# Kernel optimization log

Hardware: AMD Instinct MI355X
Metric: run time of the kernel (lower is better)

Reference implementation:

```python
import jax, jax.numpy as jnp
import numpy as np

K = 5            # srn kernel size (kernels[0])
EPSILON = 1e-3   # epsilons -> SRN additive noise scale
BN_EPS = 1e-5
NUM_SLICES = 3
OUT_CH = 64
CLASSES = 5


def _unfold(x, k):
    # torch.nn.Unfold, padding=0: (B, C*k*k, L), channel-major then (kh, kw) row-major
    B, C, H, W = x.shape
    Ho, Wo = H - k + 1, W - k + 1
    cols = jnp.stack([x[:, :, i:i + Ho, j:j + Wo]
                      for i in range(k) for j in range(k)], axis=2)  # (B,C,k*k,Ho,Wo)
    return cols.reshape(B, C * k * k, Ho * Wo), Ho, Wo


def _bn(x, g, b):
    # BatchNorm2d in training mode: batch statistics, biased variance
    m = x.mean((0, 2, 3), keepdims=True)
    v = x.var((0, 2, 3), keepdims=True)
    return (x - m) * jax.lax.rsqrt(v + BN_EPS) * g[None, :, None, None] + b[None, :, None, None]


def _conv(x, w, b):
    y = jax.lax.conv_general_dilated(x, w, (1, 1), 'VALID',
                                     dimension_numbers=('NCHW', 'OIHW', 'NCHW'))
    return y + b[None, :, None, None]


def _avgpool(x, s):
    B, C, H, W = x.shape
    return x.reshape(B, C, H // s, s, W // s, s).mean((3, 5))


def _maxpool(x, s):
    B, C, H, W = x.shape
    return x.reshape(B, C, H // s, s, W // s, s).max((3, 5))


def _srn(x, srn_w):
    B = x.shape[0]
    y, Ho, Wo = _unfold(x, K)                               # (B, n, L)
    y = y + EPSILON * jax.random.normal(jax.random.key(42), y.shape, y.dtype)
    gg = jnp.std(y, axis=1, ddof=1, keepdims=True)          # torch.std is unbiased
    y = y / gg
    O, C, _, _, S = srn_w.shape
    n = C * K * K
    X = srn_w.reshape(O, n, S)
    X = jnp.concatenate([jnp.ones((O, n, 1), X.dtype), X], axis=2)   # (O, n, S+1)
    Xcov = jnp.einsum('onf,ong->ofg', X, X)                 # X^T X, (O, 4, 4)
    Xinv = jnp.linalg.inv(Xcov)
    M = jnp.einsum('ofg,ong->ofn', Xinv, X)
    Wc = jnp.einsum('ofn,bnl->bofl', M, y)
    pred = jnp.einsum('onf,bofl->bonl', X, Wc)              # fitted values (B,O,n,L)
    err = jnp.mean((y[:, None] - pred) ** 2, axis=2)        # (B,O,L)
    err = err.reshape(B, O, Ho, Wo)
    A = (jnp.exp(-err) - np.exp(-1.0)) / (1.0 - np.exp(-1.0))
    return A - 0.5


def setup_inputs() -> dict:
    key = jax.random.key(0)
    ks = jax.random.split(key, 12)
    x = jax.random.normal(ks[0], (4, 3, 64, 64), jnp.float32)
    # xavier-style init scaled up for numerical stability of the small-matrix inverse
    srn_w = 0.05 * jax.random.normal(ks[1], (OUT_CH, 3, K, K, NUM_SLICES), jnp.float32)
    conv2_w = 0.05 * jax.random.normal(ks[2], (128, 64, 3, 3), jnp.float32)
    conv2_b = 0.01 * jax.random.normal(ks[3], (128,), jnp.float32)
    conv3_w = 0.05 * jax.random.normal(ks[4], (128, 128, 3, 3), jnp.float32)
    conv3_b = 0.01 * jax.random.normal(ks[5], (128,), jnp.float32)
    conv4_w = 0.05 * jax.random.normal(ks[6], (128, 128, 3, 3), jnp.float32)
    conv4_b = 0.01 * jax.random.normal(ks[7], (128,), jnp.float32)
    bn1_g = jnp.ones((64,), jnp.float32); bn1_b = jnp.zeros((64,), jnp.float32)
    bn2_g = jnp.ones((128,), jnp.float32); bn2_b = jnp.zeros((128,), jnp.float32)
    bn3_g = jnp.ones((128,), jnp.float32); bn3_b = jnp.zeros((128,), jnp.float32)
    bn4_g = jnp.ones((128,), jnp.float32); bn4_b = jnp.zeros((128,), jnp.float32)
    fc2_w = 0.05 * jax.random.normal(ks[8], (CLASSES, 128, 1, 1), jnp.float32)
    fc2_b = 0.01 * jax.random.normal(ks[9], (CLASSES,), jnp.float32)
    return dict(x=x, srn_w=srn_w, conv2_w=conv2_w, conv2_b=conv2_b,
                conv3_w=conv3_w, conv3_b=conv3_b, conv4_w=conv4_w, conv4_b=conv4_b,
                bn1_g=bn1_g, bn1_b=bn1_b, bn2_g=bn2_g, bn2_b=bn2_b,
                bn3_g=bn3_g, bn3_b=bn3_b, bn4_g=bn4_g, bn4_b=bn4_b,
                fc2_w=fc2_w, fc2_b=fc2_b)


def reference(x, srn_w, conv2_w, conv2_b, conv3_w, conv3_b, conv4_w, conv4_b,
              bn1_g, bn1_b, bn2_g, bn2_b, bn3_g, bn3_b, bn4_g, bn4_b,
              fc2_w, fc2_b):
    h = _srn(x, srn_w)                                      # (B,64,60,60)
    h = _avgpool(h, 2)
    h = _bn(h, bn1_g, bn1_b)
    h = jax.nn.relu(_bn(_conv(h, conv2_w, conv2_b), bn2_g, bn2_b))
    h = _avgpool(h, 2)
    h = jax.nn.relu(_bn(_conv(h, conv3_w, conv3_b), bn3_g, bn3_b))
    h = _maxpool(h, 2)
    h = jax.nn.relu(_bn(_conv(h, conv4_w, conv4_b), bn4_g, bn4_b))
    h = _maxpool(h, 4)                                      # (B,128,1,1)
    flat = h.reshape(h.shape[0], -1)                        # (B,128)
    return flat @ fc2_w.reshape(CLASSES, -1).T + fc2_b      # 1x1 conv == matmul
```

## Files before the change

### kernel.cpp

```cpp
#include <hip/hip_runtime.h>
#include <math.h>

__device__ __align__(16) float g_w2p[16 * 1152 * 4];
__device__ __align__(16) float g_w3p[32 * 1152 * 4];
__device__ __align__(16) float g_w4p[8 * 4608 * 4];
__device__ __align__(16) float g_h1[4 * 30 * 30 * 64];
__device__ __align__(16) float g_h2[4 * 14 * 14 * 4 * 128];
__device__ __align__(16) float g_h3[4 * 6 * 6 * 4 * 128];
__device__ __align__(16) float g_h4[4 * 16 * 128];

__global__ __launch_bounds__(256) void k_srn(const float* __restrict__ x,
                                             const float* __restrict__ srn_w,
                                             const float* __restrict__ w2,
                                             float* __restrict__ stats) {
    __shared__ __align__(16) float wlds[64 * 244];
    __shared__ float xsm[648];
    __shared__ float part[2 * 15 * 66];
    __shared__ float redS[256], redQ[256];
    int bid = blockIdx.x, t = threadIdx.x;
    int b = bid / 60, rem = bid % 60, r = rem >> 1, ch = rem & 1;

    for (int j = bid * 256 + t; j < 73728; j += 240 * 256) {
        int c = j & 3, s4 = j >> 2;
        int sl = s4 % 36, tmp = s4 / 36, oc_l = tmp & 31, blk = tmp >> 5;
        int it = blk & 3, ocg = blk >> 2;
        int kw = sl % 3, icq = (sl / 3) & 3, kh = sl / 12;
        int ic = it * 16 + icq * 4 + c;
        g_w2p[j] = w2[((ocg * 32 + oc_l) * 64 + ic) * 9 + kh * 3 + kw];
    }

    float4 wr[15];
#pragma unroll
    for (int k = 0; k < 15; k++) {
        int i4 = k * 256 + t;
        if (i4 < 3600) wr[k] = ((const float4*)srn_w)[i4];
    }
    float xr[3];
#pragma unroll
    for (int k = 0; k < 3; k++) {
        int i = t + k * 256;
        if (i < 648) {
            int c = i / 216, rm = i % 216, rr = rm / 36, col = rm % 36;
            int gc = ch * 30 + col; if (gc > 63) gc = 63;
            xr[k] = x[((b * 3 + c) * 64 + (2 * r + rr)) * 64 + gc];
        }
    }
#pragma unroll
    for (int k = 0; k < 15; k++) {
        int i4 = k * 256 + t;
        if (i4 < 3600) {
            float v4[4] = { wr[k].x, wr[k].y, wr[k].z, wr[k].w };
#pragma unroll
            for (int e = 0; e < 4; e++) {
                int i = i4 * 4 + e, o = i / 225, jj = i % 225;
                wlds[o * 244 + (jj / 15) * 16 + (jj % 15)] = v4[e];
            }
        }
    }
#pragma unroll
    for (int k = 0; k < 3; k++) { int i = t + k * 256; if (i < 648) xsm[i] = xr[k]; }
    __syncthreads();

    int w = t >> 6, o = t & 63;
    int rw = w & 1, cq = w >> 1, base = cq * 16;

    float z1[16], z2[16], z3[16], s[16], q[16];
#pragma unroll
    for (int i = 0; i < 16; i++) { z1[i]=0; z2[i]=0; z3[i]=0; s[i]=0; q[i]=0; }

    for (int c = 0; c < 3; c++) {
#pragma unroll
        for (int kh = 0; kh < 5; kh++) {
            float xv[20];
#pragma unroll
            for (int k = 0; k < 20; k++) xv[k] = xsm[(c * 6 + rw + kh) * 36 + base + k];
            float wf[16];
            const float* wp = &wlds[o * 244 + (c * 5 + kh) * 16];
            *(float4*)&wf[0]  = *(const float4*)&wp[0];
            *(float4*)&wf[4]  = *(const float4*)&wp[4];
            *(float4*)&wf[8]  = *(const float4*)&wp[8];
            *(float4*)&wf[12] = *(const float4*)&wp[12];
#pragma unroll
            for (int kw = 0; kw < 5; kw++) {
                float w1 = wf[kw * 3], w2v = wf[kw * 3 + 1], w3v = wf[kw * 3 + 2];
#pragma unroll
                for (int i = 0; i < 16; i++) {
                    float v = xv[kw + i];
                    s[i] += v; q[i] += v * v;
                    z1[i] += w1 * v; z2[i] += w2v * v; z3[i] += w3v * v;
                }
            }
        }
    }

    float gm[16];
    {
        float c01=0,c02=0,c03=0,c11=0,c12=0,c13=0,c22=0,c23=0,c33=0;
#pragma unroll
        for (int row = 0; row < 15; row++) {
            float wf[16];
            const float* wp = &wlds[o * 244 + row * 16];
            *(float4*)&wf[0]  = *(const float4*)&wp[0];
            *(float4*)&wf[4]  = *(const float4*)&wp[4];
            *(float4*)&wf[8]  = *(const float4*)&wp[8];
            *(float4*)&wf[12] = *(const float4*)&wp[12];
#pragma unroll
            for (int kw = 0; kw < 5; kw++) {
                float w1 = wf[kw*3], w2v = wf[kw*3+1], w3v = wf[kw*3+2];
                c01 += w1; c02 += w2v; c03 += w3v;
                c11 += w1*w1; c12 += w1*w2v; c13 += w1*w3v;
                c22 += w2v*w2v; c23 += w2v*w3v; c33 += w3v*w3v;
            }
        }
        float A[4][8];
        A[0][0]=75.f; A[0][1]=c01; A[0][2]=c02; A[0][3]=c03;
        A[1][0]=c01;  A[1][1]=c11; A[1][2]=c12; A[1][3]=c13;
        A[2][0]=c02;  A[2][1]=c12; A[2][2]=c22; A[2][3]=c23;
        A[3][0]=c03;  A[3][1]=c13; A[3][2]=c23; A[3][3]=c33;
#pragma unroll
        for (int i = 0; i < 4; i++)
#pragma unroll
            for (int j = 0; j < 4; j++) A[i][4 + j] = (i == j) ? 1.f : 0.f;
#pragma unroll
        for (int p = 0; p < 4; p++) {
            float ip = 1.f / A[p][p];
#pragma unroll
            for (int j = 0; j < 8; j++) A[p][j] *= ip;
#pragma unroll
            for (int i = 0; i < 4; i++) if (i != p) {
                float f = A[i][p];
#pragma unroll
                for (int j = 0; j < 8; j++) A[i][j] -= f * A[p][j];
            }
        }
#pragma unroll
        for (int i = 0; i < 4; i++)
#pragma unroll
            for (int j = 0; j < 4; j++) gm[i * 4 + j] = A[i][4 + j];
    }

    const float C1 = 0.36787944117144233f;
    const float INV = 1.5819767068693265f;
#pragma unroll
    for (int pp = 0; pp < 8; pp++) {
        int pl = cq * 8 + pp;
        if (pl < 15) {
            float aa = 0.f;
#pragma unroll
            for (int e = 0; e < 2; e++) {
                int i = 2 * pp + e;
                float sum = s[i], sq = q[i];
                float gg2 = (sq - sum * sum * (1.f / 75.f)) * (1.f / 74.f);
                float zf[4] = { sum, z1[i], z2[i], z3[i] };
                float qf = 0.f;
#pragma unroll
                for (int f = 0; f < 4; f++) {
                    float acc = 0.f;
#pragma unroll
                    for (int h = 0; h < 4; h++) acc += gm[f * 4 + h] * zf[h];
                    qf += acc * zf[f];
                }
                float err = (sq - qf) / (75.f * gg2);
                aa += (expf(-err) - C1) * INV - 0.5f;
            }
            part[(rw * 15 + pl) * 66 + o] = 0.25f * aa;
        }
    }
    __syncthreads();

    int j2 = t >> 6;
    float ps = 0.f, pq = 0.f;
    for (int pl = j2; pl < 15; pl += 4) {
        float v = part[pl * 66 + o] + part[(15 + pl) * 66 + o];
        g_h1[((b * 30 + r) * 30 + ch * 15 + pl) * 64 + o] = v;
        ps += v; pq += v * v;
    }
    redS[t] = ps; redQ[t] = pq;
    __syncthreads();
    if (t < 64) {
        atomicAdd(&stats[t],      redS[t] + redS[64 + t] + redS[128 + t] + redS[192 + t]);
        atomicAdd(&stats[64 + t], redQ[t] + redQ[64 + t] + redQ[128 + t] + redQ[192 + t]);
    }
}

__global__ __launch_bounds__(256) void k_conv2(const float* __restrict__ w3,
                                               const float* __restrict__ g1,
                                               const float* __restrict__ b1,
                                               float* __restrict__ stats) {
    __shared__ __align__(16) float ws[2 * 32 * 148];
    __shared__ __align__(16) float xs[3 * 16 * 64];
    __shared__ float redS[256], redQ[256];
    int blk = blockIdx.x, t = threadIdx.x;
    int b = blk / 224, rem = blk % 224, oh = rem >> 3, sub = rem & 7;
    int owh = sub >> 2, ocg = sub & 3;
    int oc_l = t & 31, grp = t >> 5;
    int now = (grp < 6) ? 2 : 1;
    int lowb = (grp < 6) ? grp * 2 : 12 + (grp - 6);

    {
        int j = blk * 256 + t;
        if (j < 147456) {
            int c = j & 3, s4 = j >> 2;
            int sl = s4 % 36, tmp = s4 / 36, oc2 = tmp & 31, bk = tmp >> 5;
            int it = bk & 7, og = bk >> 3;
            int kw = sl % 3, icq = (sl / 3) & 3, kh = sl / 12;
            int ic = it * 16 + icq * 4 + c;
            g_w3p[j] = w3[((og * 32 + oc2) * 128 + ic) * 9 + kh * 3 + kw];
        }
    }

    const float4* wsrc = (const float4*)g_w2p + (ocg * 4) * 1152;
    {
        int icb = (t & 15) * 4;
        float4 S = *(const float4*)&stats[icb], Q = *(const float4*)&stats[64 + icb];
        float4 G4 = *(const float4*)&g1[icb], B4 = *(const float4*)&b1[icb];
        float scv[4], shv[4];
        float mm[4] = { S.x, S.y, S.z, S.w }, qq[4] = { Q.x, Q.y, Q.z, Q.w };
        float gg[4] = { G4.x, G4.y, G4.z, G4.w }, bb[4] = { B4.x, B4.y, B4.z, B4.w };
#pragma unroll
        for (int c = 0; c < 4; c++) {
            float m = mm[c] * (1.f / 3600.f);
            float v = qq[c] * (1.f / 3600.f) - m * m;
            scv[c] = gg[c] * rsqrtf(v + 1e-5f);
            shv[c] = bb[c] - m * scv[c];
        }
        int px = t >> 4, ic4 = t & 15;
        float4 xr[3];
#pragma unroll
        for (int k = 0; k < 3; k++)
            xr[k] = ((const float4*)g_h1)[((b * 30 + oh + k) * 30 + owh * 14 + px) * 16 + ic4];
        float4 wreg[9];
#pragma unroll
        for (int k = 0; k < 9; k++) wreg[k] = wsrc[k * 256 + t];
#pragma unroll
        for (int k = 0; k < 3; k++) {
            float4 v;
            v.x = xr[k].x * scv[0] + shv[0]; v.y = xr[k].y * scv[1] + shv[1];
            v.z = xr[k].z * scv[2] + shv[2]; v.w = xr[k].w * scv[3] + shv[3];
            *(float4*)&xs[((k * 16 + px) * 16 + ic4) * 4] = v;
        }
#pragma unroll
        for (int k = 0; k < 9; k++) {
            int idx = k * 256 + t;
            int tile = idx / 1152, r2 = idx % 1152;
            *(float4*)&ws[tile * 4736 + (r2 / 36) * 148 + (r2 % 36) * 4] = wreg[k];
        }
    }
    __syncthreads();

    float acc[2] = {0, 0};
    for (int rr = 0; rr < 2; ++rr) {
        float4 wreg[9];
        if (rr == 0) {
#pragma unroll
            for (int k = 0; k < 9; k++) wreg[k] = wsrc[2 * 1152 + k * 256 + t];
        }
        for (int half = 0; half < 2; ++half) {
            int it = rr * 2 + half;
            const float* wB = &ws[half * 4736 + oc_l * 148];
#pragma unroll 1
            for (int icq = 0; icq < 4; icq++) {
                int xoff = it * 16 + icq * 4;
#pragma unroll
                for (int kh = 0; kh < 3; kh++) {
                    const float* wb = &wB[(kh * 4 + icq) * 12];
                    float4 w0 = *(const float4*)&wb[0];
                    float4 w1 = *(const float4*)&wb[4];
                    float4 w2v = *(const float4*)&wb[8];
                    const float* xrow = &xs[(kh * 16 + lowb) * 64 + xoff];
                    float4 x0 = *(const float4*)&xrow[0];
                    float4 x1 = *(const float4*)&xrow[64];
#pragma unroll
                    for (int i = 0; i < 2; i++) {
                        if (i < now) {
                            float4 x2 = *(const float4*)&xrow[(i + 2) * 64];
                            acc[i] += w0.x * x0.x + w0.y * x0.y + w0.z * x0.z + w0.w * x0.w
                                    + w1.x * x1.x + w1.y * x1.y + w1.z * x1.z + w1.w * x1.w
                                    + w2v.x * x2.x + w2v.y * x2.y + w2v.z * x2.z + w2v.w * x2.w;
                            x0 = x1; x1 = x2;
                        }
                    }
                }
            }
        }
        if (rr == 0) {
            __syncthreads();
#pragma unroll
            for (int k = 0; k < 9; k++) {
                int idx = k * 256 + t;
                int tile = idx / 1152, r2 = idx % 1152;
                *(float4*)&ws[tile * 4736 + (r2 / 36) * 148 + (r2 % 36) * 4] = wreg[k];
            }
            __syncthreads();
        }
    }
    int oc = ocg * 32 + oc_l;
    float ps = 0.f, pq = 0.f;
#pragma unroll
    for (int i = 0; i < 2; i++) {
        if (i < now) {
            int ow = owh * 14 + lowb + i;
            g_h2[(((b * 14 + (oh >> 1)) * 14 + (ow >> 1)) * 4 + (oh & 1) * 2 + (ow & 1)) * 128 + oc] = acc[i];
            ps += acc[i]; pq += acc[i] * acc[i];
        }
    }
    redS[t] = ps; redQ[t] = pq;
    __syncthreads();
    if (t < 32) {
        float aS = 0.f, aQ = 0.f;
#pragma unroll
        for (int k = 0; k < 8; k++) { aS += redS[t + 32 * k]; aQ += redQ[t + 32 * k]; }
        atomicAdd(&stats[128 + ocg * 32 + t], aS);
        atomicAdd(&stats[256 + ocg * 32 + t], aQ);
    }
}

__global__ __launch_bounds__(256) void k_conv3(const float* __restrict__ w4,
                                               const float* __restrict__ g2,
                                               const float* __restrict__ b2,
                                               float* __restrict__ stats) {
    __shared__ __align__(16) float ws[2 * 32 * 148];
    __shared__ __align__(16) float xs[3 * 14 * 128];
    __shared__ float redS[256], redQ[256];
    int blk = blockIdx.x, t = threadIdx.x;
    int b = blk / 48, rem = blk % 48, oh = rem >> 2, ocg = rem & 3;
    int oc_l = t & 31, grp = t >> 5;
    int now = (grp < 4) ? 2 : 1;
    int lowb = (grp < 4) ? grp * 2 : 8 + (grp - 4);

    for (int j = blk * 256 + t; j < 147456; j += 192 * 256) {
        int c = j & 3, s4 = j >> 2;
        int sl = s4 % 72, tmp = s4 / 72, oc2 = tmp & 15, blkq = tmp >> 4;
        int icq = blkq & 3, og = blkq >> 2;
        int kw = sl % 3, icb2 = (sl / 3) & 7, kh = sl / 24;
        int ic = icq * 32 + icb2 * 4 + c;
        g_w4p[j] = w4[((og * 16 + oc2) * 128 + ic) * 9 + kh * 3 + kw];
    }

    const float4* wsrc = (const float4*)g_w3p + (ocg * 8) * 1152;
    {
        int icb = (t & 31) * 4;
        float4 S = *(const float4*)&stats[128 + icb], Q = *(const float4*)&stats[256 + icb];
        float4 G4 = *(const float4*)&g2[icb], B4 = *(const float4*)&b2[icb];
        float scv[4], shv[4];
        float mm[4] = { S.x, S.y, S.z, S.w }, qq[4] = { Q.x, Q.y, Q.z, Q.w };
        float gg[4] = { G4.x, G4.y, G4.z, G4.w }, bb[4] = { B4.x, B4.y, B4.z, B4.w };
#pragma unroll
        for (int c = 0; c < 4; c++) {
            float m = mm[c] * (1.f / 3136.f);
            float v = qq[c] * (1.f / 3136.f) - m * m;
            scv[c] = gg[c] * rsqrtf(v + 1e-5f);
            shv[c] = bb[c] - m * scv[c];
        }
        float4 wreg[9];
#pragma unroll
        for (int k = 0; k < 9; k++) wreg[k] = wsrc[k * 256 + t];
        float4 pa[6], pb[6], pc[6], pd[6];
#pragma unroll
        for (int k = 0; k < 6; k++) {
            int i4 = t + k * 256;
            if (i4 < 1344) {
                int px = (i4 >> 5) % 14, rr2 = i4 / 448;
                const float4* p0 = (const float4*)&g_h2[(((b * 14 + oh + rr2) * 14 + px) * 4) * 128 + (i4 & 31) * 4];
                pa[k] = p0[0]; pb[k] = p0[32]; pc[k] = p0[64]; pd[k] = p0[96];
            }
        }
#pragma unroll
        for (int k = 0; k < 9; k++) {
            int idx = k * 256 + t;
            int tile = idx / 1152, r2 = idx % 1152;
            *(float4*)&ws[tile * 4736 + (r2 / 36) * 148 + (r2 % 36) * 4] = wreg[k];
        }
#pragma unroll
        for (int k = 0; k < 6; k++) {
            int i4 = t + k * 256;
            if (i4 < 1344) {
                float4 o4;
                o4.x = 0.25f * (fmaxf(pa[k].x * scv[0] + shv[0], 0.f) + fmaxf(pb[k].x * scv[0] + shv[0], 0.f)
                              + fmaxf(pc[k].x * scv[0] + shv[0], 0.f) + fmaxf(pd[k].x * scv[0] + shv[0], 0.f));
                o4.y = 0.25f * (fmaxf(pa[k].y * scv[1] + shv[1], 0.f) + fmaxf(pb[k].y * scv[1] + shv[1], 0.f)
                              + fmaxf(pc[k].y * scv[1] + shv[1], 0.f) + fmaxf(pd[k].y * scv[1] + shv[1], 0.f));
                o4.z = 0.25f * (fmaxf(pa[k].z * scv[2] + shv[2], 0.f) + fmaxf(pb[k].z * scv[2] + shv[2], 0.f)
                              + fmaxf(pc[k].z * scv[2] + shv[2], 0.f) + fmaxf(pd[k].z * scv[2] + shv[2], 0.f));
                o4.w = 0.25f * (fmaxf(pa[k].w * scv[3] + shv[3], 0.f) + fmaxf(pb[k].w * scv[3] + shv[3], 0.f)
                              + fmaxf(pc[k].w * scv[3] + shv[3], 0.f) + fmaxf(pd[k].w * scv[3] + shv[3], 0.f));
                *(float4*)&xs[i4 * 4] = o4;
            }
        }
    }
    __syncthreads();

    float acc[2] = {0, 0};
    for (int rr = 0; rr < 4; ++rr) {
        float4 wreg[9];
        if (rr < 3) {
#pragma unroll
            for (int k = 0; k < 9; k++) wreg[k] = wsrc[(2 * rr + 2) * 1152 + k * 256 + t];
        }
        for (int half = 0; half < 2; ++half) {
            int it = rr * 2 + half;
            const float* wB = &ws[half * 4736 + oc_l * 148];
#pragma unroll 1
            for (int icq = 0; icq < 4; icq++) {
                int xoff = it * 16 + icq * 4;
#pragma unroll
                for (int kh = 0; kh < 3; kh++) {
                    const float* wb = &wB[(kh * 4 + icq) * 12];
                    float4 w0 = *(const float4*)&wb[0];
                    float4 w1 = *(const float4*)&wb[4];
                    float4 w2v = *(const float4*)&wb[8];
                    const float* xrow = &xs[(kh * 14 + lowb) * 128 + xoff];
                    float4 x0 = *(const float4*)&xrow[0];
                    float4 x1 = *(const float4*)&xrow[128];
#pragma unroll
                    for (int i = 0; i < 2; i++) {
                        if (i < now) {
                            float4 x2 = *(const float4*)&xrow[(i + 2) * 128];
                            acc[i] += w0.x * x0.x + w0.y * x0.y + w0.z * x0.z + w0.w * x0.w
                                    + w1.x * x1.x + w1.y * x1.y + w1.z * x1.z + w1.w * x1.w
                                    + w2v.x * x2.x + w2v.y * x2.y + w2v.z * x2.z + w2v.w * x2.w;
                            x0 = x1; x1 = x2;
                        }
                    }
                }
            }
        }
        if (rr < 3) {
            __syncthreads();
#pragma unroll
            for (int k = 0; k < 9; k++) {
                int idx = k * 256 + t;
                int tile = idx / 1152, r2 = idx % 1152;
                *(float4*)&ws[tile * 4736 + (r2 / 36) * 148 + (r2 % 36) * 4] = wreg[k];
            }
            __syncthreads();
        }
    }
    int oc = ocg * 32 + oc_l;
    float ps = 0.f, pq = 0.f;
#pragma unroll
    for (int i = 0; i < 2; i++) {
        if (i < now) {
            int ow = lowb + i;
            g_h3[(((b * 6 + (oh >> 1)) * 6 + (ow >> 1)) * 4 + (oh & 1) * 2 + (ow & 1)) * 128 + oc] = acc[i];
            ps += acc[i]; pq += acc[i] * acc[i];
        }
    }
    redS[t] = ps; redQ[t] = pq;
    __syncthreads();
    if (t < 32) {
        float aS = 0.f, aQ = 0.f;
#pragma unroll
        for (int k = 0; k < 8; k++) { aS += redS[t + 32 * k]; aQ += redQ[t + 32 * k]; }
        atomicAdd(&stats[384 + ocg * 32 + t], aS);
        atomicAdd(&stats[512 + ocg * 32 + t], aQ);
    }
}

__global__ __launch_bounds__(256) void k_conv4(const float* __restrict__ g3,
                                               const float* __restrict__ b3,
                                               float* __restrict__ stats) {
    __shared__ __align__(16) float ws[64 * 292];
    __shared__ __align__(16) float xs[3 * 6 * 128];
    __shared__ float red[256];
    int blk = blockIdx.x, t = threadIdx.x;
    int b = blk / 32, rem = blk % 32, oh = rem / 8, ocg = rem % 8;
    int oc_l = t & 15, ow = (t >> 4) & 3, icq = t >> 6;

    {
        int icb = (t & 31) * 4;
        float4 S = *(const float4*)&stats[384 + icb], Q = *(const float4*)&stats[512 + icb];
        float4 G4 = *(const float4*)&g3[icb], B4 = *(const float4*)&b3[icb];
        float scv[4], shv[4];
        float mm[4] = { S.x, S.y, S.z, S.w }, qq[4] = { Q.x, Q.y, Q.z, Q.w };
        float gg[4] = { G4.x, G4.y, G4.z, G4.w }, bb[4] = { B4.x, B4.y, B4.z, B4.w };
#pragma unroll
        for (int c = 0; c < 4; c++) {
            float m = mm[c] * (1.f / 576.f);
            float v = qq[c] * (1.f / 576.f) - m * m;
            scv[c] = gg[c] * rsqrtf(v + 1e-5f);
            shv[c] = bb[c] - m * scv[c];
        }
        const float4* wsrc = (const float4*)g_w4p + ocg * 4608;
        float4 wreg[18];
#pragma unroll
        for (int k = 0; k < 18; k++) wreg[k] = wsrc[k * 256 + t];
        float4 pa[3], pb[3], pc[3], pd[3];
#pragma unroll
        for (int k = 0; k < 3; k++) {
            int i4 = t + k * 256;
            if (i4 < 576) {
                int px = (i4 >> 5) % 6, rr = i4 / 192;
                const float4* p0 = (const float4*)&g_h3[(((b * 6 + oh + rr) * 6 + px) * 4) * 128 + (i4 & 31) * 4];
                pa[k] = p0[0]; pb[k] = p0[32]; pc[k] = p0[64]; pd[k] = p0[96];
            }
        }
#pragma unroll
        for (int k = 0; k < 18; k++) {
            int idx = k * 256 + t;
            *(float4*)&ws[(idx / 72) * 292 + (idx % 72) * 4] = wreg[k];
        }
#pragma unroll
        for (int k = 0; k < 3; k++) {
            int i4 = t + k * 256;
            if (i4 < 576) {
                float4 o4;
                o4.x = fmaxf(fmaxf(fmaxf(pa[k].x * scv[0] + shv[0], pb[k].x * scv[0] + shv[0]),
                                   fmaxf(pc[k].x * scv[0] + shv[0], pd[k].x * scv[0] + shv[0])), 0.f);
                o4.y = fmaxf(fmaxf(fmaxf(pa[k].y * scv[1] + shv[1], pb[k].y * scv[1] + shv[1]),
                                   fmaxf(pc[k].y * scv[1] + shv[1], pd[k].y * scv[1] + shv[1])), 0.f);
                o4.z = fmaxf(fmaxf(fmaxf(pa[k].z * scv[2] + shv[2], pb[k].z * scv[2] + shv[2]),
                                   fmaxf(pc[k].z * scv[2] + shv[2], pd[k].z * scv[2] + shv[2])), 0.f);
                o4.w = fmaxf(fmaxf(fmaxf(pa[k].w * scv[3] + shv[3], pb[k].w * scv[3] + shv[3]),
                                   fmaxf(pc[k].w * scv[3] + shv[3], pd[k].w * scv[3] + shv[3])), 0.f);
                *(float4*)&xs[i4 * 4] = o4;
            }
        }
    }
    __syncthreads();

    float acc = 0.f;
    const float* wbase = &ws[(icq * 16 + oc_l) * 292];
#pragma unroll 1
    for (int icbq = 0; icbq < 8; icbq++) {
#pragma unroll
        for (int kh = 0; kh < 3; kh++) {
            const float* wb = &wbase[(kh * 8 + icbq) * 12];
            float4 w0 = *(const float4*)&wb[0];
            float4 w1 = *(const float4*)&wb[4];
            float4 w2v = *(const float4*)&wb[8];
            float4 x0 = *(const float4*)&xs[(kh * 6 + ow) * 128 + icq * 32 + icbq * 4];
            float4 x1 = *(const float4*)&xs[(kh * 6 + ow + 1) * 128 + icq * 32 + icbq * 4];
            float4 x2 = *(const float4*)&xs[(kh * 6 + ow + 2) * 128 + icq * 32 + icbq * 4];
            acc += w0.x * x0.x + w0.y * x0.y + w0.z * x0.z + w0.w * x0.w
                 + w1.x * x1.x + w1.y * x1.y + w1.z * x1.z + w1.w * x1.w
                 + w2v.x * x2.x + w2v.y * x2.y + w2v.z * x2.z + w2v.w * x2.w;
        }
    }
    red[t] = acc;
    __syncthreads();
    if (t < 64) {
        float v = red[t] + red[t + 64] + red[t + 128] + red[t + 192];
        int oc = ocg * 16 + (t & 15);
        g_h4[((b * 4 + oh) * 4 + (t >> 4)) * 128 + oc] = v;
        float ps = v + __shfl_xor(v, 16);  ps += __shfl_xor(ps, 32);
        float pv = v * v;
        float pq = pv + __shfl_xor(pv, 16); pq += __shfl_xor(pq, 32);
        if (t < 16) {
            atomicAdd(&stats[640 + ocg * 16 + t], ps);
            atomicAdd(&stats[768 + ocg * 16 + t], pq);
        }
    }
}

__global__ __launch_bounds__(256) void k_final(const float* __restrict__ g4,
                                               const float* __restrict__ b4,
                                               const float* __restrict__ fcw,
                                               const float* __restrict__ fcb,
                                               const float* __restrict__ stats,
                                               float* __restrict__ out) {
    __shared__ float sc[128], sh[128];
    __shared__ float pooled[4][128];
    int t = threadIdx.x;
    if (t < 128) {
        float m = stats[640 + t] * (1.f / 64.f);
        float v = stats[768 + t] * (1.f / 64.f) - m * m;
        float rs = rsqrtf(v + 1e-5f);
        sc[t] = g4[t] * rs; sh[t] = b4[t] - m * sc[t];
    }
    __syncthreads();
    for (int item = t; item < 512; item += 256) {
        int bb = item >> 7, oc = item & 127;
        float s = sc[oc], h = sh[oc];
        float mx = 0.f;
#pragma unroll
        for (int k = 0; k < 16; k++) mx = fmaxf(mx, g_h4[(bb * 16 + k) * 128 + oc] * s + h);
        pooled[bb][oc] = mx;
    }
    __syncthreads();
    if (t < 20) {
        int bb = t / 5, cls = t % 5;
        float acc = fcb[cls];
        const float* w = &fcw[cls * 128];
        for (int oc = 0; oc < 128; oc++) acc += pooled[bb][oc] * w[oc];
        out[bb * 5 + cls] = acc;
    }
}

extern "C" void kernel_launch(void* const* d_in, const int* in_sizes, int n_in,
                              void* d_out, int out_size, void* d_ws, size_t ws_size,
                              hipStream_t stream) {
    (void)in_sizes; (void)n_in; (void)out_size; (void)ws_size;
    const float* x     = (const float*)d_in[0];
    const float* srn_w = (const float*)d_in[1];
    const float* w2    = (const float*)d_in[2];
    const float* w3    = (const float*)d_in[4];
    const float* w4    = (const float*)d_in[6];
    const float* g1 = (const float*)d_in[8];  const float* b1 = (const float*)d_in[9];
    const float* g2 = (const float*)d_in[10]; const float* b2 = (const float*)d_in[11];
    const float* g3 = (const float*)d_in[12]; const float* b3 = (const float*)d_in[13];
    const float* g4 = (const float*)d_in[14]; const float* b4 = (const float*)d_in[15];
    const float* fcw = (const float*)d_in[16]; const float* fcb = (const float*)d_in[17];
    float* out = (float*)d_out;
    float* stats = (float*)d_ws;

    hipMemsetAsync(d_ws, 0, 4096, stream);
    k_srn  <<<dim3(240), dim3(256), 0, stream>>>(x, srn_w, w2, stats);
    k_conv2<<<dim3(896), dim3(256), 0, stream>>>(w3, g1, b1, stats);
    k_conv3<<<dim3(192), dim3(256), 0, stream>>>(w4, g2, b2, stats);
    k_conv4<<<dim3(128), dim3(256), 0, stream>>>(g3, b3, stats);
    k_final<<<dim3(1),   dim3(256), 0, stream>>>(g4, b4, fcw, fcb, stats, out);
}
```

Before: 102.3 us.

## Split conv3 input-channel reduction across two thread halves and fold final into conv4

```diff
diff --git a/kernel.cpp b/kernel.cpp
--- a/kernel.cpp
+++ b/kernel.cpp
@@ -315,20 +315,21 @@
     }
 }
 
-__global__ __launch_bounds__(256) void k_conv3(const float* __restrict__ w4,
+__global__ __launch_bounds__(512) void k_conv3(const float* __restrict__ w4,
                                                const float* __restrict__ g2,
                                                const float* __restrict__ b2,
                                                float* __restrict__ stats) {
     __shared__ __align__(16) float ws[2 * 32 * 148];
     __shared__ __align__(16) float xs[3 * 14 * 128];
-    __shared__ float redS[256], redQ[256];
+    __shared__ float accr[512 * 2];
+    __shared__ float redS[512], redQ[512];
     int blk = blockIdx.x, t = threadIdx.x;
     int b = blk / 48, rem = blk % 48, oh = rem >> 2, ocg = rem & 3;
-    int oc_l = t & 31, grp = t >> 5;
+    int oc_l = t & 31, icqh = (t >> 5) & 1, grp = t >> 6;
     int now = (grp < 4) ? 2 : 1;
     int lowb = (grp < 4) ? grp * 2 : 8 + (grp - 4);
 
-    for (int j = blk * 256 + t; j < 147456; j += 192 * 256) {
+    for (int j = blk * 512 + t; j < 147456; j += 192 * 512) {
         int c = j & 3, s4 = j >> 2;
         int sl = s4 % 72, tmp = s4 / 72, oc2 = tmp & 15, blkq = tmp >> 4;
         int icq = blkq & 3, og = blkq >> 2;
@@ -352,13 +353,13 @@
             scv[c] = gg[c] * rsqrtf(v + 1e-5f);
             shv[c] = bb[c] - m * scv[c];
         }
-        float4 wreg[9];
-#pragma unroll
-        for (int k = 0; k < 9; k++) wreg[k] = wsrc[k * 256 + t];
-        float4 pa[6], pb[6], pc[6], pd[6];
-#pragma unroll
-        for (int k = 0; k < 6; k++) {
-            int i4 = t + k * 256;
+        float4 wreg[5];
+#pragma unroll
+        for (int k = 0; k < 5; k++) { int i4 = k * 512 + t; if (i4 < 2304) wreg[k] = wsrc[i4]; }
+        float4 pa[3], pb[3], pc[3], pd[3];
+#pragma unroll
+        for (int k = 0; k < 3; k++) {
+            int i4 = t + k * 512;
             if (i4 < 1344) {
                 int px = (i4 >> 5) % 14, rr2 = i4 / 448;
                 const float4* p0 = (const float4*)&g_h2[(((b * 14 + oh + rr2) * 14 + px) * 4) * 128 + (i4 & 31) * 4];
@@ -366,14 +367,16 @@
             }
         }
 #pragma unroll
-        for (int k = 0; k < 9; k++) {
-            int idx = k * 256 + t;
-            int tile = idx / 1152, r2 = idx % 1152;
-            *(float4*)&ws[tile * 4736 + (r2 / 36) * 148 + (r2 % 36) * 4] = wreg[k];
-        }
-#pragma unroll
-        for (int k = 0; k < 6; k++) {
-            int i4 = t + k * 256;
+        for (int k = 0; k < 5; k++) {
+            int i4 = k * 512 + t;
+            if (i4 < 2304) {
+                int tile = i4 / 1152, r2 = i4 % 1152;
+                *(float4*)&ws[tile * 4736 + (r2 / 36) * 148 + (r2 % 36) * 4] = wreg[k];
+            }
+        }
+#pragma unroll
+        for (int k = 0; k < 3; k++) {
+            int i4 = t + k * 512;
             if (i4 < 1344) {
                 float4 o4;
                 o4.x = 0.25f * (fmaxf(pa[k].x * scv[0] + shv[0], 0.f) + fmaxf(pb[k].x * scv[0] + shv[0], 0.f)
@@ -392,16 +395,17 @@
 
     float acc[2] = {0, 0};
     for (int rr = 0; rr < 4; ++rr) {
-        float4 wreg[9];
+        float4 wreg[5];
         if (rr < 3) {
 #pragma unroll
-            for (int k = 0; k < 9; k++) wreg[k] = wsrc[(2 * rr + 2) * 1152 + k * 256 + t];
+            for (int k = 0; k < 5; k++) { int i4 = k * 512 + t; if (i4 < 2304) wreg[k] = wsrc[(2 * rr + 2) * 1152 + i4]; }
         }
         for (int half = 0; half < 2; ++half) {
             int it = rr * 2 + half;
             const float* wB = &ws[half * 4736 + oc_l * 148];
 #pragma unroll 1
-            for (int icq = 0; icq < 4; icq++) {
+            for (int iq = 0; iq < 2; iq++) {
+                int icq = icqh * 2 + iq;
                 int xoff = it * 16 + icq * 4;
 #pragma unroll
                 for (int kh = 0; kh < 3; kh++) {
@@ -428,22 +432,31 @@
         if (rr < 3) {
             __syncthreads();
 #pragma unroll
-            for (int k = 0; k < 9; k++) {
-                int idx = k * 256 + t;
-                int tile = idx / 1152, r2 = idx % 1152;
-                *(float4*)&ws[tile * 4736 + (r2 / 36) * 148 + (r2 % 36) * 4] = wreg[k];
+            for (int k = 0; k < 5; k++) {
+                int i4 = k * 512 + t;
+                if (i4 < 2304) {
+                    int tile = i4 / 1152, r2 = i4 % 1152;
+                    *(float4*)&ws[tile * 4736 + (r2 / 36) * 148 + (r2 % 36) * 4] = wreg[k];
+                }
             }
             __syncthreads();
         }
     }
-    int oc = ocg * 32 + oc_l;
+    accr[t * 2]     = acc[0];
+    accr[t * 2 + 1] = acc[1];
+    __syncthreads();
     float ps = 0.f, pq = 0.f;
-#pragma unroll
-    for (int i = 0; i < 2; i++) {
-        if (i < now) {
-            int ow = lowb + i;
-            g_h3[(((b * 6 + (oh >> 1)) * 6 + (ow >> 1)) * 4 + (oh & 1) * 2 + (ow & 1)) * 128 + oc] = acc[i];
-            ps += acc[i]; pq += acc[i] * acc[i];
+    if (icqh == 0) {
+        acc[0] += accr[(t + 32) * 2];
+        acc[1] += accr[(t + 32) * 2 + 1];
+        int oc = ocg * 32 + oc_l;
+#pragma unroll
+        for (int i = 0; i < 2; i++) {
+            if (i < now) {
+                int ow = lowb + i;
+                g_h3[(((b * 6 + (oh >> 1)) * 6 + (ow >> 1)) * 4 + (oh & 1) * 2 + (ow & 1)) * 128 + oc] = acc[i];
+                ps += acc[i]; pq += acc[i] * acc[i];
+            }
         }
     }
     redS[t] = ps; redQ[t] = pq;
@@ -451,7 +464,7 @@
     if (t < 32) {
         float aS = 0.f, aQ = 0.f;
 #pragma unroll
-        for (int k = 0; k < 8; k++) { aS += redS[t + 32 * k]; aQ += redQ[t + 32 * k]; }
+        for (int k = 0; k < 16; k++) { aS += redS[t + 32 * k]; aQ += redQ[t + 32 * k]; }
         atomicAdd(&stats[384 + ocg * 32 + t], aS);
         atomicAdd(&stats[512 + ocg * 32 + t], aQ);
     }
@@ -459,7 +472,12 @@
 
 __global__ __launch_bounds__(256) void k_conv4(const float* __restrict__ g3,
                                                const float* __restrict__ b3,
-                                               float* __restrict__ stats) {
+                                               const float* __restrict__ g4,
+                                               const float* __restrict__ b4,
+                                               const float* __restrict__ fcw,
+                                               const float* __restrict__ fcb,
+                                               float* __restrict__ stats,
+                                               float* __restrict__ out) {
     __shared__ __align__(16) float ws[64 * 292];
     __shared__ __align__(16) float xs[3 * 6 * 128];
     __shared__ float red[256];
@@ -551,39 +569,41 @@
             atomicAdd(&stats[768 + ocg * 16 + t], pq);
         }
     }
-}
-
-__global__ __launch_bounds__(256) void k_final(const float* __restrict__ g4,
-                                               const float* __restrict__ b4,
-                                               const float* __restrict__ fcw,
-                                               const float* __restrict__ fcb,
-                                               const float* __restrict__ stats,
-                                               float* __restrict__ out) {
-    __shared__ float sc[128], sh[128];
-    __shared__ float pooled[4][128];
-    int t = threadIdx.x;
-    if (t < 128) {
-        float m = stats[640 + t] * (1.f / 64.f);
-        float v = stats[768 + t] * (1.f / 64.f) - m * m;
-        float rs = rsqrtf(v + 1e-5f);
-        sc[t] = g4[t] * rs; sh[t] = b4[t] - m * sc[t];
-    }
-    __syncthreads();
-    for (int item = t; item < 512; item += 256) {
-        int bb = item >> 7, oc = item & 127;
-        float s = sc[oc], h = sh[oc];
-        float mx = 0.f;
-#pragma unroll
-        for (int k = 0; k < 16; k++) mx = fmaxf(mx, g_h4[(bb * 16 + k) * 128 + oc] * s + h);
-        pooled[bb][oc] = mx;
-    }
-    __syncthreads();
-    if (t < 20) {
-        int bb = t / 5, cls = t % 5;
-        float acc = fcb[cls];
-        const float* w = &fcw[cls * 128];
-        for (int oc = 0; oc < 128; oc++) acc += pooled[bb][oc] * w[oc];
-        out[bb * 5 + cls] = acc;
+
+    __threadfence();
+    __shared__ int lastFlag;
+    if (t == 0) {
+        int prev = atomicAdd((int*)stats + 896, 1);
+        lastFlag = (prev == (int)gridDim.x - 1);
+    }
+    __syncthreads();
+    if (lastFlag) {
+        __threadfence();
+        __shared__ float sc[128], sh[128];
+        __shared__ float pooled[4][128];
+        if (t < 128) {
+            float m = stats[640 + t] * (1.f / 64.f);
+            float v = stats[768 + t] * (1.f / 64.f) - m * m;
+            float rs = rsqrtf(v + 1e-5f);
+            sc[t] = g4[t] * rs; sh[t] = b4[t] - m * sc[t];
+        }
+        __syncthreads();
+        for (int item = t; item < 512; item += 256) {
+            int bb = item >> 7, oc = item & 127;
+            float s = sc[oc], h = sh[oc];
+            float mx = 0.f;
+#pragma unroll
+            for (int k = 0; k < 16; k++) mx = fmaxf(mx, g_h4[(bb * 16 + k) * 128 + oc] * s + h);
+            pooled[bb][oc] = mx;
+        }
+        __syncthreads();
+        if (t < 20) {
+            int bb = t / 5, cls = t % 5;
+            float a2 = fcb[cls];
+            const float* w = &fcw[cls * 128];
+            for (int oc = 0; oc < 128; oc++) a2 += pooled[bb][oc] * w[oc];
+            out[bb * 5 + cls] = a2;
+        }
     }
 }
 
@@ -607,7 +627,6 @@
     hipMemsetAsync(d_ws, 0, 4096, stream);
     k_srn  <<<dim3(240), dim3(256), 0, stream>>>(x, srn_w, w2, stats);
     k_conv2<<<dim3(896), dim3(256), 0, stream>>>(w3, g1, b1, stats);
-    k_conv3<<<dim3(192), dim3(256), 0, stream>>>(w4, g2, b2, stats);
-    k_conv4<<<dim3(128), dim3(256), 0, stream>>>(g3, b3, stats);
-    k_final<<<dim3(1),   dim3(256), 0, stream>>>(g4, b4, fcw, fcb, stats, out);
+    k_conv3<<<dim3(192), dim3(512), 0, stream>>>(w4, g2, b2, stats);
+    k_conv4<<<dim3(128), dim3(256), 0, stream>>>(g3, b3, g4, b4, fcw, fcb, stats, out);
 }
```

New measurement: 106.5 us. 1.04x slower.
